# Kernel tuning notes

Measured on AMD Instinct MI355X. Metric: run time of the kernel, lower is better.

Reference implementation:

```python
import jax, jax.numpy as jnp
import numpy as np

# HT config: input_shape = output_shape = (8,8,8,8), rank = 8, d = 4 modes
B = 4096
M = 8      # per-mode input dim
N = 8      # per-mode output dim
R = 8      # HT rank
FEAT = M ** 4  # 4096


def setup_inputs() -> dict:
    key = jax.random.key(0)
    ks = jax.random.split(key, 8)
    x = jax.random.normal(ks[0], (B, FEAT), dtype=jnp.float32)
    # leaf factors: (in_p, out_p, rank); xavier-style scale over the input mode
    f_std = np.float32(np.sqrt(2.0 / (M + N * R)))
    F0 = jax.random.normal(ks[1], (M, N, R), dtype=jnp.float32) * f_std
    F1 = jax.random.normal(ks[2], (M, N, R), dtype=jnp.float32) * f_std
    F2 = jax.random.normal(ks[3], (M, N, R), dtype=jnp.float32) * f_std
    F3 = jax.random.normal(ks[4], (M, N, R), dtype=jnp.float32) * f_std
    # internal cores: (left_rank, right_rank, parent_rank)
    c_std = np.float32(np.sqrt(2.0 / (R + R * R)))
    CL = jax.random.normal(ks[5], (R, R, R), dtype=jnp.float32) * c_std
    CR = jax.random.normal(ks[6], (R, R, R), dtype=jnp.float32) * c_std
    bound = np.float32(1.0 / np.sqrt(FEAT))
    bias = jax.random.uniform(ks[7], (FEAT,), dtype=jnp.float32, minval=-bound, maxval=bound)
    return {"x": x, "F0": F0, "F1": F1, "F2": F2, "F3": F3,
            "CL": CL, "CR": CR, "bias": bias}


def reference(x, F0, F1, F2, F3, CL, CR, bias):
    b = x.shape[0]
    # (b, i, j, k, l): one axis per HT mode
    x4 = x.reshape(b, M, M, M, M)
    # Pre-contract each subtree's two leaves with its core (tiny tensors):
    # left transfer  W_L[i, j, a, c, p], right transfer W_R[k, l, d, e, p].
    # This is the same tensor-network contraction as the tn.Node graph,
    # just in an efficient associativity order.
    WL = jnp.einsum('iar,jcs,rsp->ijacp', F0, F1, CL)
    WR = jnp.einsum('kdr,les,rsp->kldep', F2, F3, CR)
    # contract left subtree against the input: (b, k, l, a, c, p)
    yL = jnp.einsum('bijkl,ijacp->bklacp', x4, WL)
    # contract right subtree; parent edges of the two subtrees are joined (p)
    y = jnp.einsum('bklacp,kldep->bacde', yL, WR)
    return y.reshape(b, FEAT) + bias
```

## Files before the change

### kernel.cpp

```cpp
#include <hip/hip_runtime.h>
#include <hip/hip_bf16.h>


typedef short bf16x8 __attribute__((ext_vector_type(8)));
typedef float f32x16 __attribute__((ext_vector_type(16)));

union Frag8 {
    bf16x8 v;
    unsigned int u4[4];
};

static __device__ __forceinline__ unsigned int pkbf(float a, float b) {
    __hip_bfloat162 h = __float22bfloat162_rn(float2{a, b});
    return *reinterpret_cast<unsigned int*>(&h);
}

static __device__ __forceinline__ unsigned short f2bf(float f) {
    unsigned int u = __float_as_uint(f);
    u = (u + 0x7FFFu + ((u >> 16) & 1u)) >> 16;
    return (unsigned short)u;
}

__global__ void ht_precompute(const float* __restrict__ F0, const float* __restrict__ F1,
                              const float* __restrict__ F2, const float* __restrict__ F3,
                              const float* __restrict__ CL, const float* __restrict__ CR,
                              unsigned short* __restrict__ frags) {
    int idx = blockIdx.x * blockDim.x + threadIdx.x;
    int isW  = idx >> 15;
    int r15  = idx & 32767;
    int p    = r15 >> 12;
    int t    = (r15 >> 11) & 1;
    int kc   = (r15 >> 9) & 3;
    int lane = (r15 >> 3) & 63;
    int j    = r15 & 7;
    int n = t * 32 + (lane & 31);
    int k = kc * 16 + ((lane >> 5) & 1) * 8 + j;
    const float* Fa = isW ? F2 : F0;
    const float* Fb = isW ? F3 : F1;
    const float* C  = isW ? CR : CL;
    int i1 = k >> 3, i2 = k & 7, o1 = n >> 3, o2 = n & 7;
    float acc = 0.f;
    for (int r = 0; r < 8; ++r) {
        float fa = Fa[(i1 * 8 + o1) * 8 + r];
        for (int s = 0; s < 8; ++s)
            acc += fa * Fb[(i2 * 8 + o2) * 8 + s] * C[(r * 8 + s) * 8 + p];
    }
    frags[(size_t)isW * 32768 + ((((p * 2 + t) * 4 + kc) << 6) + lane) * 8 + j] = f2bf(acc);
}

#define Y_PITCH 66

__global__ __launch_bounds__(256, 2) void ht_main(const float* __restrict__ x,
                                                  const unsigned short* __restrict__ frags,
                                                  const float* __restrict__ bias,
                                                  float* __restrict__ out) {
    __shared__ float Ybuf[4][32 * Y_PITCH];
    const int tid  = threadIdx.x;
    const int lane = tid & 63;
    const int w    = __builtin_amdgcn_readfirstlane(tid >> 6);
    const int b    = blockIdx.x * 4 + w;
    const int l31  = lane & 31;
    const int hi   = lane >> 5;

    Frag8 xf[2][4];
    const float* xb = x + ((size_t)b << 12);
#pragma unroll
    for (int rb = 0; rb < 2; ++rb)
#pragma unroll
        for (int kc = 0; kc < 4; ++kc) {
            const float* src = xb + (kc * 16 + hi * 8) * 64 + rb * 32 + l31;
#pragma unroll
            for (int j = 0; j < 8; j += 2)
                xf[rb][kc].u4[j >> 1] = pkbf(src[j * 64], src[(j + 1) * 64]);
        }

    f32x16 acc[2][2];
#pragma unroll
    for (int i = 0; i < 2; ++i)
#pragma unroll
        for (int j = 0; j < 2; ++j)
#pragma unroll
            for (int e = 0; e < 16; ++e)
                acc[i][j][e] = 0.f;

    const unsigned short* AF = frags;
    const unsigned short* WF = frags + 32768;

#pragma unroll 2
    for (int p = 0; p < 8; ++p) {
        Frag8 af[2][4], wf[2][4];
#pragma unroll
        for (int t = 0; t < 2; ++t)
#pragma unroll
            for (int kc = 0; kc < 4; ++kc) {
                int off = (((p * 2 + t) * 4 + kc) << 9) + lane * 8;
                af[t][kc].v = *(const bf16x8*)(AF + off);
                wf[t][kc].v = *(const bf16x8*)(WF + off);
            }
#pragma unroll
        for (int rb = 0; rb < 2; ++rb) {
#pragma unroll
            for (int cb = 0; cb < 2; ++cb) {
                f32x16 t;
#pragma unroll
                for (int e = 0; e < 16; ++e) t[e] = 0.f;
#pragma unroll
                for (int kc = 0; kc < 4; ++kc)
                    t = __builtin_amdgcn_mfma_f32_32x32x16_bf16(xf[rb][kc].v, af[cb][kc].v, t, 0, 0, 0);
                unsigned int wd[8];
#pragma unroll
                for (int h = 0; h < 8; ++h) wd[h] = pkbf(t[2 * h], t[2 * h + 1]);
                auto s02 = __builtin_amdgcn_permlane32_swap(wd[0], wd[2], false, false);
                auto s13 = __builtin_amdgcn_permlane32_swap(wd[1], wd[3], false, false);
                auto s46 = __builtin_amdgcn_permlane32_swap(wd[4], wd[6], false, false);
                auto s57 = __builtin_amdgcn_permlane32_swap(wd[5], wd[7], false, false);
                Frag8 tb0, tb1;
                tb0.u4[0] = s02[0]; tb0.u4[1] = s13[0]; tb0.u4[2] = s02[1]; tb0.u4[3] = s13[1];
                tb1.u4[0] = s46[0]; tb1.u4[1] = s57[0]; tb1.u4[2] = s46[1]; tb1.u4[3] = s57[1];
                acc[0][cb] = __builtin_amdgcn_mfma_f32_32x32x16_bf16(wf[0][2 * rb].v,     tb0.v, acc[0][cb], 0, 0, 0);
                acc[0][cb] = __builtin_amdgcn_mfma_f32_32x32x16_bf16(wf[0][2 * rb + 1].v, tb1.v, acc[0][cb], 0, 0, 0);
                acc[1][cb] = __builtin_amdgcn_mfma_f32_32x32x16_bf16(wf[1][2 * rb].v,     tb0.v, acc[1][cb], 0, 0, 0);
                acc[1][cb] = __builtin_amdgcn_mfma_f32_32x32x16_bf16(wf[1][2 * rb + 1].v, tb1.v, acc[1][cb], 0, 0, 0);
            }
        }
    }

    float* Yw = &Ybuf[w][0];
    float* ob = out + ((size_t)b << 12);
#pragma unroll
    for (int cb = 0; cb < 2; ++cb) {
#pragma unroll
        for (int mt = 0; mt < 2; ++mt)
#pragma unroll
            for (int rp = 0; rp < 8; ++rp) {
                int de = mt * 32 + 8 * (rp >> 1) + 2 * (rp & 1) + 4 * hi;
                float2 v;
                v.x = acc[mt][cb][2 * rp];
                v.y = acc[mt][cb][2 * rp + 1];
                *(float2*)(&Yw[l31 * Y_PITCH + de]) = v;
            }
#pragma unroll
        for (int i = 0; i < 16; ++i) {
            int acl = 2 * i + hi;
            float2 v = *(float2*)(&Yw[acl * Y_PITCH + 2 * l31]);
            int o = (cb * 32 + acl) * 64 + 2 * l31;
            float2 bv = *(const float2*)(bias + o);
            v.x += bv.x;
            v.y += bv.y;
            *(float2*)(ob + o) = v;
        }
    }
}

extern "C" void kernel_launch(void* const* d_in, const int* in_sizes, int n_in,
                              void* d_out, int out_size, void* d_ws, size_t ws_size,
                              hipStream_t stream) {
    const float* x    = (const float*)d_in[0];
    const float* F0   = (const float*)d_in[1];
    const float* F1   = (const float*)d_in[2];
    const float* F2   = (const float*)d_in[3];
    const float* F3   = (const float*)d_in[4];
    const float* CL   = (const float*)d_in[5];
    const float* CR   = (const float*)d_in[6];
    const float* bias = (const float*)d_in[7];
    float* out = (float*)d_out;
    unsigned short* frags = (unsigned short*)d_ws;

    const int B = in_sizes[0] / 4096;

    ht_precompute<<<256, 256, 0, stream>>>(F0, F1, F2, F3, CL, CR, frags);
    ht_main<<<B / 4, 256, 0, stream>>>(x, frags, bias, out);
}
```

Measured before the change: 153.8 us.

## Stage weight fragments through LDS with double-buffered async loads; factor precompute

The main kernel now shares each per-p slice of the precomputed A/W fragments across the four waves in a block. Each wave issues asynchronous global-to-LDS loads for its quarter of the slice, double-buffered so the next slice is in flight while the current one feeds the MFMAs. This replaces per-wave global loads of the full fragment set. The precompute kernel is also refactored into two staged contractions in shared memory over 16 blocks instead of a brute-force triple loop per element. The cost is two block barriers per p iteration and a larger shared-memory footprint, which may affect occupancy.

Result: faster. 147.6 us (-4.1%).

```diff
diff --git a/kernel.cpp b/kernel.cpp
--- a/kernel.cpp
+++ b/kernel.cpp
@@ -15,37 +15,60 @@
     return *reinterpret_cast<unsigned int*>(&h);
 }
 
-static __device__ __forceinline__ unsigned short f2bf(float f) {
-    unsigned int u = __float_as_uint(f);
-    u = (u + 0x7FFFu + ((u >> 16) & 1u)) >> 16;
-    return (unsigned short)u;
-}
-
-__global__ void ht_precompute(const float* __restrict__ F0, const float* __restrict__ F1,
-                              const float* __restrict__ F2, const float* __restrict__ F3,
-                              const float* __restrict__ CL, const float* __restrict__ CR,
-                              unsigned short* __restrict__ frags) {
-    int idx = blockIdx.x * blockDim.x + threadIdx.x;
-    int isW  = idx >> 15;
-    int r15  = idx & 32767;
-    int p    = r15 >> 12;
-    int t    = (r15 >> 11) & 1;
-    int kc   = (r15 >> 9) & 3;
-    int lane = (r15 >> 3) & 63;
-    int j    = r15 & 7;
-    int n = t * 32 + (lane & 31);
-    int k = kc * 16 + ((lane >> 5) & 1) * 8 + j;
+__global__ __launch_bounds__(256) void ht_precompute(
+        const float* __restrict__ F0, const float* __restrict__ F1,
+        const float* __restrict__ F2, const float* __restrict__ F3,
+        const float* __restrict__ CL, const float* __restrict__ CR,
+        unsigned short* __restrict__ frags) {
+    __shared__ float sFa[512], sFb[512], sC[512], sG[512];
+    const int isW = blockIdx.x >> 3;
+    const int p   = blockIdx.x & 7;
     const float* Fa = isW ? F2 : F0;
     const float* Fb = isW ? F3 : F1;
     const float* C  = isW ? CR : CL;
-    int i1 = k >> 3, i2 = k & 7, o1 = n >> 3, o2 = n & 7;
-    float acc = 0.f;
-    for (int r = 0; r < 8; ++r) {
-        float fa = Fa[(i1 * 8 + o1) * 8 + r];
+    const int tid = threadIdx.x;
+
+    for (int u = tid; u < 512; u += 256) {
+        sFa[u] = Fa[u]; sFb[u] = Fb[u]; sC[u] = C[u];
+    }
+    __syncthreads();
+
+#pragma unroll
+    for (int e = 0; e < 2; ++e) {
+        int u = tid + e * 256;
+        int r = u >> 6, jc = u & 63;
+        float acc = 0.f;
+#pragma unroll
         for (int s = 0; s < 8; ++s)
-            acc += fa * Fb[(i2 * 8 + o2) * 8 + s] * C[(r * 8 + s) * 8 + p];
-    }
-    frags[(size_t)isW * 32768 + ((((p * 2 + t) * 4 + kc) << 6) + lane) * 8 + j] = f2bf(acc);
+            acc += sFb[jc * 8 + s] * sC[(r * 8 + s) * 8 + p];
+        sG[u] = acc;
+    }
+    __syncthreads();
+
+#pragma unroll
+    for (int e = 0; e < 2; ++e) {
+        int g  = tid + e * 256;
+        int i1 = g >> 6, n = g & 63;
+        int a  = n >> 3, c = n & 7;
+        float fa[8];
+#pragma unroll
+        for (int r = 0; r < 8; ++r) fa[r] = sFa[(i1 * 8 + a) * 8 + r];
+        unsigned int pk[4];
+#pragma unroll
+        for (int jp = 0; jp < 4; ++jp) {
+            float o0 = 0.f, o1 = 0.f;
+#pragma unroll
+            for (int r = 0; r < 8; ++r) {
+                o0 += fa[r] * sG[r * 64 + (2 * jp) * 8 + c];
+                o1 += fa[r] * sG[r * 64 + (2 * jp + 1) * 8 + c];
+            }
+            pk[jp] = pkbf(o0, o1);
+        }
+        int t = n >> 5, kc = i1 >> 1, lane_ = (i1 & 1) * 32 + (n & 31);
+        unsigned int* dst = (unsigned int*)(frags + (size_t)isW * 32768 +
+                                            ((((p * 2 + t) * 4 + kc) << 6) + lane_) * 8);
+        *(uint4*)dst = uint4{pk[0], pk[1], pk[2], pk[3]};
+    }
 }
 
 #define Y_PITCH 66
@@ -54,7 +77,7 @@
                                                   const unsigned short* __restrict__ frags,
                                                   const float* __restrict__ bias,
                                                   float* __restrict__ out) {
-    __shared__ float Ybuf[4][32 * Y_PITCH];
+    __shared__ __align__(16) char smem[34816];
     const int tid  = threadIdx.x;
     const int lane = tid & 63;
     const int w    = __builtin_amdgcn_readfirstlane(tid >> 6);
@@ -83,19 +106,41 @@
             for (int e = 0; e < 16; ++e)
                 acc[i][j][e] = 0.f;
 
-    const unsigned short* AF = frags;
-    const unsigned short* WF = frags + 32768;
-
-#pragma unroll 2
+    auto stage_issue = [&](int buf, int pn) {
+        const char* gA = (const char*)frags + pn * 8192 + w * 2048 + lane * 16;
+        const char* gW = (const char*)frags + 65536 + pn * 8192 + w * 2048 + lane * 16;
+        char* lA = smem + buf * 16384 + w * 2048;
+        char* lW = smem + buf * 16384 + 8192 + w * 2048;
+        __builtin_amdgcn_global_load_lds((const __attribute__((address_space(1))) void*)gA,
+                                         (__attribute__((address_space(3))) void*)lA, 16, 0, 0);
+        __builtin_amdgcn_global_load_lds((const __attribute__((address_space(1))) void*)(gA + 1024),
+                                         (__attribute__((address_space(3))) void*)(lA + 1024), 16, 0, 0);
+        __builtin_amdgcn_global_load_lds((const __attribute__((address_space(1))) void*)gW,
+                                         (__attribute__((address_space(3))) void*)lW, 16, 0, 0);
+        __builtin_amdgcn_global_load_lds((const __attribute__((address_space(1))) void*)(gW + 1024),
+                                         (__attribute__((address_space(3))) void*)(lW + 1024), 16, 0, 0);
+    };
+
+    stage_issue(0, 0);
+
+#pragma unroll
     for (int p = 0; p < 8; ++p) {
+        if (p < 7) {
+            stage_issue((p + 1) & 1, p + 1);
+            asm volatile("s_waitcnt vmcnt(4)" ::: "memory");
+        } else {
+            asm volatile("s_waitcnt vmcnt(0)" ::: "memory");
+        }
+        __builtin_amdgcn_s_barrier();
+
+        const unsigned short* LB = (const unsigned short*)(smem + (p & 1) * 16384);
         Frag8 af[2][4], wf[2][4];
 #pragma unroll
         for (int t = 0; t < 2; ++t)
 #pragma unroll
             for (int kc = 0; kc < 4; ++kc) {
-                int off = (((p * 2 + t) * 4 + kc) << 9) + lane * 8;
-                af[t][kc].v = *(const bf16x8*)(AF + off);
-                wf[t][kc].v = *(const bf16x8*)(WF + off);
+                af[t][kc].v = *(const bf16x8*)(LB + (t * 4 + kc) * 512 + lane * 8);
+                wf[t][kc].v = *(const bf16x8*)(LB + 4096 + (t * 4 + kc) * 512 + lane * 8);
             }
 #pragma unroll
         for (int rb = 0; rb < 2; ++rb) {
@@ -123,9 +168,10 @@
                 acc[1][cb] = __builtin_amdgcn_mfma_f32_32x32x16_bf16(wf[1][2 * rb + 1].v, tb1.v, acc[1][cb], 0, 0, 0);
             }
         }
-    }
-
-    float* Yw = &Ybuf[w][0];
+        __builtin_amdgcn_s_barrier();
+    }
+
+    float* Yw = (float*)smem + w * (32 * Y_PITCH);
     float* ob = out + ((size_t)b << 12);
 #pragma unroll
     for (int cb = 0; cb < 2; ++cb) {
@@ -168,6 +214,6 @@
 
     const int B = in_sizes[0] / 4096;
 
-    ht_precompute<<<256, 256, 0, stream>>>(F0, F1, F2, F3, CL, CR, frags);
+    ht_precompute<<<16, 256, 0, stream>>>(F0, F1, F2, F3, CL, CR, frags);
     ht_main<<<B / 4, 256, 0, stream>>>(x, frags, bias, out);
 }
```
